# Kernel tuning notes

Measured on AMD Instinct MI355X. Metric: run time of the kernel, lower is better.

## Reference

```python
import jax, jax.numpy as jnp
import numpy as np

B, S, D, E, K = 4, 4096, 2048, 64, 2


def setup_inputs() -> dict:
    key = jax.random.key(0)
    k1, k2 = jax.random.split(key)
    hidden_states = jax.random.normal(k1, (B, S, D), dtype=jnp.float32)
    gate_weight = jax.random.normal(k2, (E, D), dtype=jnp.float32) * 0.02
    return {"hidden_states": hidden_states, "gate_weight": gate_weight}


def reference(hidden_states, gate_weight):
    b, s, d = hidden_states.shape
    e = gate_weight.shape[0]
    n = b * s
    x = hidden_states.reshape(n, d)
    logits = x @ gate_weight.T                                  # [N, E]
    # Original reassigns gate_logits = softmax(gate_logits) in fp32.
    probs = jax.nn.softmax(logits.astype(jnp.float32), axis=-1)  # [N, E]

    top_v, top_i = jax.lax.top_k(probs, K)                       # [N, K]
    top_k_gates = top_v  # normalize_gate_prob_before_dropping=False

    oh = jax.nn.one_hot(top_i, e, dtype=probs.dtype)             # [N, K, E]
    gates = jnp.einsum('nke,nk->ne', oh, top_k_gates)            # scatter of top-k gates

    # Auxiliary losses (training path, use_aux_loss=True)
    gates_mean = gates.mean(axis=0)                              # [E]
    selection_mean = oh.sum(axis=(0, 1)) / n                     # [E]
    load_balancing_loss = (gates_mean * selection_mean).sum() * e
    # NOTE: original computes z-loss on the softmaxed probs (gate_logits was overwritten)
    router_z_loss = (jax.nn.logsumexp(probs, axis=-1) ** 2).mean()

    # torch scatter_ with index [B,S,1,1] only ever writes slot k=0.
    dispatch0 = oh.sum(axis=1).reshape(b, s, e)                  # 1.0 at top-k experts
    combine0 = gates.reshape(b, s, e)
    pad = ((0, 0), (0, 0), (0, 0), (0, K - 1))
    dispatch_tensor = jnp.pad(dispatch0[..., None], pad)         # [B,S,E,K]
    combine_tensor = jnp.pad(combine0[..., None], pad)           # [B,S,E,K]

    return dispatch_tensor, combine_tensor, load_balancing_loss, router_z_loss
```

## Files before the change

### kernel.cpp

```cpp
#include <hip/hip_runtime.h>
#include <hip/hip_bf16.h>
#include <cstddef>

namespace {
constexpr int kD = 2048;
constexpr int kE = 64;
constexpr int kN = 16384;
constexpr size_t kDispatchFloats = (size_t)kN * kE * 2;
constexpr size_t kWsplitOff = 1024;
}

typedef short short8_t __attribute__((ext_vector_type(8)));
typedef float f32x4 __attribute__((ext_vector_type(4)));

__global__ void zero_ws_kernel(float* __restrict__ ws) {
  ws[threadIdx.x] = 0.0f;
}

__device__ __forceinline__ void split3(float f, unsigned short& s1,
                                       unsigned short& s2, unsigned short& s3) {
  __hip_bfloat16 h1 = __float2bfloat16(f);
  float r1 = (f - __bfloat162float(h1)) * 256.0f;
  __hip_bfloat16 h2 = __float2bfloat16(r1);
  float r2 = (r1 - __bfloat162float(h2)) * 256.0f;
  __hip_bfloat16 h3 = __float2bfloat16(r2);
  s1 = __builtin_bit_cast(unsigned short, h1);
  s2 = __builtin_bit_cast(unsigned short, h2);
  s3 = __builtin_bit_cast(unsigned short, h3);
}

__global__ __launch_bounds__(256)
void split_w_kernel(const float* __restrict__ W, unsigned short* __restrict__ img) {
  const int t   = blockIdx.x * 256 + threadIdx.x;
  const int dq  = t >> 12;
  const int c   = (t >> 9) & 7;
  const int row = (t >> 3) & 63;
  const int cs8 = t & 7;
  const int co  = cs8 ^ (row & 7);
  const float* src = W + (size_t)row * kD + dq * 512 + c * 64 + co * 8;
  const float4 v0 = *reinterpret_cast<const float4*>(src);
  const float4 v1 = *reinterpret_cast<const float4*>(src + 4);
  short8_t o1, o2, o3;
  unsigned short s1, s2, s3;
  split3(v0.x, s1, s2, s3); o1[0]=(short)s1; o2[0]=(short)s2; o3[0]=(short)s3;
  split3(v0.y, s1, s2, s3); o1[1]=(short)s1; o2[1]=(short)s2; o3[1]=(short)s3;
  split3(v0.z, s1, s2, s3); o1[2]=(short)s1; o2[2]=(short)s2; o3[2]=(short)s3;
  split3(v0.w, s1, s2, s3); o1[3]=(short)s1; o2[3]=(short)s2; o3[3]=(short)s3;
  split3(v1.x, s1, s2, s3); o1[4]=(short)s1; o2[4]=(short)s2; o3[4]=(short)s3;
  split3(v1.y, s1, s2, s3); o1[5]=(short)s1; o2[5]=(short)s2; o3[5]=(short)s3;
  split3(v1.z, s1, s2, s3); o1[6]=(short)s1; o2[6]=(short)s2; o3[6]=(short)s3;
  split3(v1.w, s1, s2, s3); o1[7]=(short)s1; o2[7]=(short)s2; o3[7]=(short)s3;
  unsigned short* dst = img + (size_t)(dq * 8 + c) * 12288 + row * 64 + cs8 * 8;
  *reinterpret_cast<short8_t*>(dst + 0 * 4096) = o1;
  *reinterpret_cast<short8_t*>(dst + 1 * 4096) = o2;
  *reinterpret_cast<short8_t*>(dst + 2 * 4096) = o3;
}

__device__ __forceinline__ void conv_store8(float4 a, float4 b,
                                            unsigned short (*dst)[64][64],
                                            int row, int seg) {
  short8_t o1, o2, o3;
  unsigned short s1, s2, s3;
  split3(a.x, s1, s2, s3); o1[0]=(short)s1; o2[0]=(short)s2; o3[0]=(short)s3;
  split3(a.y, s1, s2, s3); o1[1]=(short)s1; o2[1]=(short)s2; o3[1]=(short)s3;
  split3(a.z, s1, s2, s3); o1[2]=(short)s1; o2[2]=(short)s2; o3[2]=(short)s3;
  split3(a.w, s1, s2, s3); o1[3]=(short)s1; o2[3]=(short)s2; o3[3]=(short)s3;
  split3(b.x, s1, s2, s3); o1[4]=(short)s1; o2[4]=(short)s2; o3[4]=(short)s3;
  split3(b.y, s1, s2, s3); o1[5]=(short)s1; o2[5]=(short)s2; o3[5]=(short)s3;
  split3(b.z, s1, s2, s3); o1[6]=(short)s1; o2[6]=(short)s2; o3[6]=(short)s3;
  split3(b.w, s1, s2, s3); o1[7]=(short)s1; o2[7]=(short)s2; o3[7]=(short)s3;
  const int col = seg ^ (row & 7);
  *reinterpret_cast<short8_t*>(&dst[0][row][col * 8]) = o1;
  *reinterpret_cast<short8_t*>(&dst[1][row][col * 8]) = o2;
  *reinterpret_cast<short8_t*>(&dst[2][row][col * 8]) = o3;
}

__global__ __launch_bounds__(512)
void logits_kernel(const float* __restrict__ x,
                   const unsigned short* __restrict__ wimg,
                   float* __restrict__ out) {
  __shared__ unsigned short xs[3][64][64];
  __shared__ unsigned short wt[3][64][64];

  const int tid  = threadIdx.x;
  const int lane = tid & 63;
  const int wv   = __builtin_amdgcn_readfirstlane(tid >> 6);
  const int wr   = wv >> 2;
  const int wc   = (wv >> 1) & 1;
  const int kh   = wv & 1;
  const int tile = blockIdx.x & 255;
  const int dq   = blockIdx.x >> 8;
  const int lrow = lane & 15;
  const int lk   = lane >> 4;

  const int row = tid >> 3, seg = tid & 7;
  const float4* __restrict__ bx = reinterpret_cast<const float4*>(x) +
      ((size_t)tile * 64 + row) * 512 + dq * 128 + seg * 2;
  const unsigned short* __restrict__ wbase =
      wimg + (size_t)dq * 8 * 12288 + tid * 8;
  unsigned short* wtf = &wt[0][0][0];

  f32x4 acc0[2][2], acc1[2][2], acc2[2][2];
  const f32x4 z4 = {0.0f, 0.0f, 0.0f, 0.0f};
#pragma unroll
  for (int a = 0; a < 2; ++a)
#pragma unroll
    for (int b = 0; b < 2; ++b) { acc0[a][b] = z4; acc1[a][b] = z4; acc2[a][b] = z4; }

  float4 vx0 = bx[0], vx1 = bx[1];

  for (int c = 0; c < 8; ++c) {
    const unsigned short* wsrc = wbase + (size_t)c * 12288;
#pragma unroll
    for (int i = 0; i < 3; ++i)
      __builtin_amdgcn_global_load_lds(
          (const __attribute__((address_space(1))) void*)(wsrc + i * 4096),
          (__attribute__((address_space(3))) void*)(wtf + i * 4096 + wv * 512),
          16, 0, 0);
    __builtin_amdgcn_sched_barrier(0);
    const float4 xa = vx0, xb = vx1;
    const int cn = (c + 1) & 7;
    vx0 = bx[cn * 16 + 0];
    vx1 = bx[cn * 16 + 1];
    conv_store8(xa, xb, xs, row, seg);
    asm volatile("s_waitcnt vmcnt(2) lgkmcnt(0)" ::: "memory");
    __builtin_amdgcn_sched_barrier(0);
    __builtin_amdgcn_s_barrier();
    __builtin_amdgcn_sched_barrier(0);
    {
      const int kc = kh * 4 + lk;
      short8_t a1[2], a2[2], a3[2], b1[2], b2[2], b3[2];
#pragma unroll
      for (int nt = 0; nt < 2; ++nt) {
        const int e = wc * 32 + nt * 16 + lrow;
        const int cw = (kc ^ (e & 7)) * 8;
        b1[nt] = *reinterpret_cast<const short8_t*>(&wt[0][e][cw]);
        b2[nt] = *reinterpret_cast<const short8_t*>(&wt[1][e][cw]);
        b3[nt] = *reinterpret_cast<const short8_t*>(&wt[2][e][cw]);
      }
#pragma unroll
      for (int mt = 0; mt < 2; ++mt) {
        const int r = wr * 32 + mt * 16 + lrow;
        const int cw = (kc ^ (r & 7)) * 8;
        a1[mt] = *reinterpret_cast<const short8_t*>(&xs[0][r][cw]);
        a2[mt] = *reinterpret_cast<const short8_t*>(&xs[1][r][cw]);
        a3[mt] = *reinterpret_cast<const short8_t*>(&xs[2][r][cw]);
      }
#pragma unroll
      for (int mt = 0; mt < 2; ++mt)
#pragma unroll
        for (int nt = 0; nt < 2; ++nt) {
          acc0[mt][nt] = __builtin_amdgcn_mfma_f32_16x16x32_bf16(a1[mt], b1[nt], acc0[mt][nt], 0, 0, 0);
          acc1[mt][nt] = __builtin_amdgcn_mfma_f32_16x16x32_bf16(a1[mt], b2[nt], acc1[mt][nt], 0, 0, 0);
          acc1[mt][nt] = __builtin_amdgcn_mfma_f32_16x16x32_bf16(a2[mt], b1[nt], acc1[mt][nt], 0, 0, 0);
          acc2[mt][nt] = __builtin_amdgcn_mfma_f32_16x16x32_bf16(a1[mt], b3[nt], acc2[mt][nt], 0, 0, 0);
          acc2[mt][nt] = __builtin_amdgcn_mfma_f32_16x16x32_bf16(a3[mt], b1[nt], acc2[mt][nt], 0, 0, 0);
          acc2[mt][nt] = __builtin_amdgcn_mfma_f32_16x16x32_bf16(a2[mt], b2[nt], acc2[mt][nt], 0, 0, 0);
        }
    }
    __builtin_amdgcn_sched_barrier(0);
    __builtin_amdgcn_s_barrier();
  }

  const float k8 = 1.0f / 256.0f, k16 = 1.0f / 65536.0f;
  float* __restrict__ mbuf = reinterpret_cast<float*>(&xs[0][0][0]);
  if (kh == 1) {
#pragma unroll
    for (int mt = 0; mt < 2; ++mt)
#pragma unroll
      for (int nt = 0; nt < 2; ++nt)
#pragma unroll
        for (int r = 0; r < 4; ++r) {
          const int trow = wr * 32 + mt * 16 + lk * 4 + r;
          const int col  = wc * 32 + nt * 16 + lrow;
          mbuf[trow * 65 + col] =
              acc0[mt][nt][r] + acc1[mt][nt][r] * k8 + acc2[mt][nt][r] * k16;
        }
  }
  __syncthreads();
  if (kh == 0) {
    float* __restrict__ base = out + ((dq < 2) ? (size_t)0 : kDispatchFloats);
#pragma unroll
    for (int mt = 0; mt < 2; ++mt)
#pragma unroll
      for (int r = 0; r < 4; ++r) {
        const int trow = wr * 32 + mt * 16 + lk * 4 + r;
        const size_t n = (size_t)tile * 64 + trow;
        float* __restrict__ dst =
            base + n * 128 + (dq & 1) * 64 + wc * 32 + lrow;
#pragma unroll
        for (int nt = 0; nt < 2; ++nt) {
          const int col = wc * 32 + nt * 16 + lrow;
          dst[nt * 16] = acc0[mt][nt][r] + acc1[mt][nt][r] * k8 +
                         acc2[mt][nt][r] * k16 + mbuf[trow * 65 + col];
        }
      }
  }
}

__global__ __launch_bounds__(256)
void gate_kernel(float* __restrict__ out, float* __restrict__ ws) {
  __shared__ float lg[64][65];
  __shared__ int ti0[64], ti1[64];
  __shared__ float tv0[64], tv1[64], tz2[64];
  const int tid  = threadIdx.x;
  const int tile = blockIdx.x;

  float* __restrict__ outd = out + (size_t)tile * 8192;
  float* __restrict__ outc = out + kDispatchFloats + (size_t)tile * 8192;
  const float4* __restrict__ d4 = reinterpret_cast<const float4*>(outd);
  const float4* __restrict__ c4 = reinterpret_cast<const float4*>(outc);

  const int tq = tid >> 4, q = tid & 15;
#pragma unroll
  for (int k = 0; k < 4; ++k) {
    const int t = k * 16 + tq;
    const float4 a = d4[t * 32 + q];
    const float4 b = d4[t * 32 + 16 + q];
    const float4 c = c4[t * 32 + q];
    const float4 d = c4[t * 32 + 16 + q];
    lg[t][q * 4 + 0] = a.x + b.x + c.x + d.x;
    lg[t][q * 4 + 1] = a.y + b.y + c.y + d.y;
    lg[t][q * 4 + 2] = a.z + b.z + c.z + d.z;
    lg[t][q * 4 + 3] = a.w + b.w + c.w + d.w;
  }
  __syncthreads();

  if (tid < 64) {
    float v0 = -INFINITY, v1 = -INFINITY;
    int i0 = 0, i1 = 0;
    for (int e = 0; e < kE; ++e) {
      const float l = lg[tid][e];
      if (l > v0) { v1 = v0; i1 = i0; v0 = l; i0 = e; }
      else if (l > v1) { v1 = l; i1 = e; }
    }
    const float m = v0;
    float s = 0.0f;
    for (int e = 0; e < kE; ++e) s += __expf(lg[tid][e] - m);
    const float rs = 1.0f / s;
    float zexp = 0.0f;
    for (int e = 0; e < kE; ++e) zexp += __expf(__expf(lg[tid][e] - m) * rs);
    const float z = logf(zexp);
    ti0[tid] = i0; ti1[tid] = i1;
    tv0[tid] = rs;
    tv1[tid] = __expf(v1 - m) * rs;
    tz2[tid] = z * z;
  }
  __syncthreads();

  if (tid < kE) {
    float g = 0.0f, cnt = 0.0f;
    for (int t = 0; t < 64; ++t) {
      if (ti0[t] == tid) { g += tv0[t]; cnt += 1.0f; }
      if (ti1[t] == tid) { g += tv1[t]; cnt += 1.0f; }
    }
    atomicAdd(&ws[tid], g);
    atomicAdd(&ws[kE + tid], cnt);
    float z2 = tz2[tid];
    for (int off = 32; off; off >>= 1) z2 += __shfl_down(z2, off);
    if (tid == 0) atomicAdd(&ws[2 * kE], z2);
  }

  {
    const int t = tid >> 2, sub = tid & 3;
    const int i0 = ti0[t], i1 = ti1[t];
    const float v0 = tv0[t], v1 = tv1[t];
    float4* __restrict__ dp = reinterpret_cast<float4*>(outd) + t * 32;
    float4* __restrict__ cp = reinterpret_cast<float4*>(outc) + t * 32;
#pragma unroll
    for (int j = 0; j < 8; ++j) {
      const int qq = sub * 8 + j;
      const int e0 = qq * 2, e1 = qq * 2 + 1;
      const float d0v = (e0 == i0 || e0 == i1) ? 1.0f : 0.0f;
      const float d1v = (e1 == i0 || e1 == i1) ? 1.0f : 0.0f;
      const float c0 = (e0 == i0) ? v0 : ((e0 == i1) ? v1 : 0.0f);
      const float c1 = (e1 == i0) ? v0 : ((e1 == i1) ? v1 : 0.0f);
      dp[qq] = make_float4(d0v, 0.0f, d1v, 0.0f);
      cp[qq] = make_float4(c0, 0.0f, c1, 0.0f);
    }
  }
}

__global__ void finalize_kernel(const float* __restrict__ ws,
                                float* __restrict__ out) {
  const int e = threadIdx.x;
  float prod = ws[e] * ws[kE + e];
  for (int off = 32; off; off >>= 1) prod += __shfl_down(prod, off);
  if (e == 0) {
    const size_t base = kDispatchFloats * 2;
    const float invN = 1.0f / (float)kN;
    out[base]     = prod * ((float)kE * invN * invN);
    out[base + 1] = ws[2 * kE] * invN;
  }
}

extern "C" void kernel_launch(void* const* d_in, const int* in_sizes, int n_in,
                              void* d_out, int out_size, void* d_ws,
                              size_t ws_size, hipStream_t stream) {
  const float* x = (const float*)d_in[0];
  const float* W = (const float*)d_in[1];
  float* out = (float*)d_out;
  float* ws = (float*)d_ws;
  unsigned short* wimg = (unsigned short*)(ws + kWsplitOff);

  zero_ws_kernel<<<1, 256, 0, stream>>>(ws);
  split_w_kernel<<<64, 256, 0, stream>>>(W, wimg);
  logits_kernel<<<1024, 512, 0, stream>>>(x, wimg, out);
  gate_kernel<<<256, 256, 0, stream>>>(out, ws);
  finalize_kernel<<<1, kE, 0, stream>>>(ws, out);
}
```

Before: 73.29 us.

## Stage fp32 x in LDS, split per wave, single accumulator, fuse zero-init

```diff
diff --git a/kernel.cpp b/kernel.cpp
--- a/kernel.cpp
+++ b/kernel.cpp
@@ -13,25 +13,33 @@
 typedef short short8_t __attribute__((ext_vector_type(8)));
 typedef float f32x4 __attribute__((ext_vector_type(4)));
 
-__global__ void zero_ws_kernel(float* __restrict__ ws) {
-  ws[threadIdx.x] = 0.0f;
-}
-
 __device__ __forceinline__ void split3(float f, unsigned short& s1,
                                        unsigned short& s2, unsigned short& s3) {
   __hip_bfloat16 h1 = __float2bfloat16(f);
-  float r1 = (f - __bfloat162float(h1)) * 256.0f;
+  float r1 = f - __bfloat162float(h1);
   __hip_bfloat16 h2 = __float2bfloat16(r1);
-  float r2 = (r1 - __bfloat162float(h2)) * 256.0f;
+  float r2 = r1 - __bfloat162float(h2);
   __hip_bfloat16 h3 = __float2bfloat16(r2);
   s1 = __builtin_bit_cast(unsigned short, h1);
   s2 = __builtin_bit_cast(unsigned short, h2);
   s3 = __builtin_bit_cast(unsigned short, h3);
 }
 
+__device__ __forceinline__ void split8(f32x4 a, f32x4 b, short8_t& o1,
+                                       short8_t& o2, short8_t& o3) {
+  unsigned short s1, s2, s3;
+#define SP(v, i, j) \
+  split3((v)[i], s1, s2, s3); o1[j]=(short)s1; o2[j]=(short)s2; o3[j]=(short)s3;
+  SP(a, 0, 0) SP(a, 1, 1) SP(a, 2, 2) SP(a, 3, 3)
+  SP(b, 0, 4) SP(b, 1, 5) SP(b, 2, 6) SP(b, 3, 7)
+#undef SP
+}
+
 __global__ __launch_bounds__(256)
-void split_w_kernel(const float* __restrict__ W, unsigned short* __restrict__ img) {
-  const int t   = blockIdx.x * 256 + threadIdx.x;
+void prep_kernel(const float* __restrict__ W, unsigned short* __restrict__ img,
+                 float* __restrict__ ws) {
+  const int t = blockIdx.x * 256 + threadIdx.x;
+  if (t < 512) ws[t] = 0.0f;
   const int dq  = t >> 12;
   const int c   = (t >> 9) & 7;
   const int row = (t >> 3) & 63;
@@ -56,31 +64,14 @@
   *reinterpret_cast<short8_t*>(dst + 2 * 4096) = o3;
 }
 
-__device__ __forceinline__ void conv_store8(float4 a, float4 b,
-                                            unsigned short (*dst)[64][64],
-                                            int row, int seg) {
-  short8_t o1, o2, o3;
-  unsigned short s1, s2, s3;
-  split3(a.x, s1, s2, s3); o1[0]=(short)s1; o2[0]=(short)s2; o3[0]=(short)s3;
-  split3(a.y, s1, s2, s3); o1[1]=(short)s1; o2[1]=(short)s2; o3[1]=(short)s3;
-  split3(a.z, s1, s2, s3); o1[2]=(short)s1; o2[2]=(short)s2; o3[2]=(short)s3;
-  split3(a.w, s1, s2, s3); o1[3]=(short)s1; o2[3]=(short)s2; o3[3]=(short)s3;
-  split3(b.x, s1, s2, s3); o1[4]=(short)s1; o2[4]=(short)s2; o3[4]=(short)s3;
-  split3(b.y, s1, s2, s3); o1[5]=(short)s1; o2[5]=(short)s2; o3[5]=(short)s3;
-  split3(b.z, s1, s2, s3); o1[6]=(short)s1; o2[6]=(short)s2; o3[6]=(short)s3;
-  split3(b.w, s1, s2, s3); o1[7]=(short)s1; o2[7]=(short)s2; o3[7]=(short)s3;
-  const int col = seg ^ (row & 7);
-  *reinterpret_cast<short8_t*>(&dst[0][row][col * 8]) = o1;
-  *reinterpret_cast<short8_t*>(&dst[1][row][col * 8]) = o2;
-  *reinterpret_cast<short8_t*>(&dst[2][row][col * 8]) = o3;
-}
-
-__global__ __launch_bounds__(512)
+__global__ __launch_bounds__(512, 4)
 void logits_kernel(const float* __restrict__ x,
                    const unsigned short* __restrict__ wimg,
                    float* __restrict__ out) {
-  __shared__ unsigned short xs[3][64][64];
-  __shared__ unsigned short wt[3][64][64];
+  __shared__ __attribute__((aligned(16))) unsigned char smem[40960];
+  float* xsf = reinterpret_cast<float*>(smem);
+  unsigned short (*wt)[64][64] =
+      reinterpret_cast<unsigned short (*)[64][64]>(smem + 16384);
 
   const int tid  = threadIdx.x;
   const int lane = tid & 63;
@@ -99,13 +90,12 @@
   const unsigned short* __restrict__ wbase =
       wimg + (size_t)dq * 8 * 12288 + tid * 8;
   unsigned short* wtf = &wt[0][0][0];
-
-  f32x4 acc0[2][2], acc1[2][2], acc2[2][2];
+  const int sc0 = ((2 * seg) ^ (row & 15)) * 4;
+  const int sc1 = ((2 * seg + 1) ^ (row & 15)) * 4;
+
+  f32x4 acc[2][2];
   const f32x4 z4 = {0.0f, 0.0f, 0.0f, 0.0f};
-#pragma unroll
-  for (int a = 0; a < 2; ++a)
-#pragma unroll
-    for (int b = 0; b < 2; ++b) { acc0[a][b] = z4; acc1[a][b] = z4; acc2[a][b] = z4; }
+  acc[0][0] = z4; acc[0][1] = z4; acc[1][0] = z4; acc[1][1] = z4;
 
   float4 vx0 = bx[0], vx1 = bx[1];
 
@@ -122,14 +112,15 @@
     const int cn = (c + 1) & 7;
     vx0 = bx[cn * 16 + 0];
     vx1 = bx[cn * 16 + 1];
-    conv_store8(xa, xb, xs, row, seg);
+    *reinterpret_cast<float4*>(xsf + row * 64 + sc0) = xa;
+    *reinterpret_cast<float4*>(xsf + row * 64 + sc1) = xb;
     asm volatile("s_waitcnt vmcnt(2) lgkmcnt(0)" ::: "memory");
     __builtin_amdgcn_sched_barrier(0);
     __builtin_amdgcn_s_barrier();
     __builtin_amdgcn_sched_barrier(0);
     {
       const int kc = kh * 4 + lk;
-      short8_t a1[2], a2[2], a3[2], b1[2], b2[2], b3[2];
+      short8_t b1[2], b2[2], b3[2];
 #pragma unroll
       for (int nt = 0; nt < 2; ++nt) {
         const int e = wc * 32 + nt * 16 + lrow;
@@ -140,30 +131,29 @@
       }
 #pragma unroll
       for (int mt = 0; mt < 2; ++mt) {
-        const int r = wr * 32 + mt * 16 + lrow;
-        const int cw = (kc ^ (r & 7)) * 8;
-        a1[mt] = *reinterpret_cast<const short8_t*>(&xs[0][r][cw]);
-        a2[mt] = *reinterpret_cast<const short8_t*>(&xs[1][r][cw]);
-        a3[mt] = *reinterpret_cast<const short8_t*>(&xs[2][r][cw]);
+        const int ra = wr * 32 + mt * 16 + lrow;
+        const int ca0 = ((2 * kc) ^ (ra & 15)) * 4;
+        const int ca1 = ((2 * kc + 1) ^ (ra & 15)) * 4;
+        const f32x4 va = *reinterpret_cast<const f32x4*>(xsf + ra * 64 + ca0);
+        const f32x4 vb = *reinterpret_cast<const f32x4*>(xsf + ra * 64 + ca1);
+        short8_t a1, a2, a3;
+        split8(va, vb, a1, a2, a3);
+#pragma unroll
+        for (int nt = 0; nt < 2; ++nt) {
+          acc[mt][nt] = __builtin_amdgcn_mfma_f32_16x16x32_bf16(a1, b1[nt], acc[mt][nt], 0, 0, 0);
+          acc[mt][nt] = __builtin_amdgcn_mfma_f32_16x16x32_bf16(a1, b2[nt], acc[mt][nt], 0, 0, 0);
+          acc[mt][nt] = __builtin_amdgcn_mfma_f32_16x16x32_bf16(a2, b1[nt], acc[mt][nt], 0, 0, 0);
+          acc[mt][nt] = __builtin_amdgcn_mfma_f32_16x16x32_bf16(a1, b3[nt], acc[mt][nt], 0, 0, 0);
+          acc[mt][nt] = __builtin_amdgcn_mfma_f32_16x16x32_bf16(a3, b1[nt], acc[mt][nt], 0, 0, 0);
+          acc[mt][nt] = __builtin_amdgcn_mfma_f32_16x16x32_bf16(a2, b2[nt], acc[mt][nt], 0, 0, 0);
+        }
       }
-#pragma unroll
-      for (int mt = 0; mt < 2; ++mt)
-#pragma unroll
-        for (int nt = 0; nt < 2; ++nt) {
-          acc0[mt][nt] = __builtin_amdgcn_mfma_f32_16x16x32_bf16(a1[mt], b1[nt], acc0[mt][nt], 0, 0, 0);
-          acc1[mt][nt] = __builtin_amdgcn_mfma_f32_16x16x32_bf16(a1[mt], b2[nt], acc1[mt][nt], 0, 0, 0);
-          acc1[mt][nt] = __builtin_amdgcn_mfma_f32_16x16x32_bf16(a2[mt], b1[nt], acc1[mt][nt], 0, 0, 0);
-          acc2[mt][nt] = __builtin_amdgcn_mfma_f32_16x16x32_bf16(a1[mt], b3[nt], acc2[mt][nt], 0, 0, 0);
-          acc2[mt][nt] = __builtin_amdgcn_mfma_f32_16x16x32_bf16(a3[mt], b1[nt], acc2[mt][nt], 0, 0, 0);
-          acc2[mt][nt] = __builtin_amdgcn_mfma_f32_16x16x32_bf16(a2[mt], b2[nt], acc2[mt][nt], 0, 0, 0);
-        }
     }
     __builtin_amdgcn_sched_barrier(0);
     __builtin_amdgcn_s_barrier();
   }
 
-  const float k8 = 1.0f / 256.0f, k16 = 1.0f / 65536.0f;
-  float* __restrict__ mbuf = reinterpret_cast<float*>(&xs[0][0][0]);
+  float* __restrict__ mbuf = reinterpret_cast<float*>(smem + 16384);
   if (kh == 1) {
 #pragma unroll
     for (int mt = 0; mt < 2; ++mt)
@@ -173,8 +163,7 @@
         for (int r = 0; r < 4; ++r) {
           const int trow = wr * 32 + mt * 16 + lk * 4 + r;
           const int col  = wc * 32 + nt * 16 + lrow;
-          mbuf[trow * 65 + col] =
-              acc0[mt][nt][r] + acc1[mt][nt][r] * k8 + acc2[mt][nt][r] * k16;
+          mbuf[trow * 65 + col] = acc[mt][nt][r];
         }
   }
   __syncthreads();
@@ -191,8 +180,7 @@
 #pragma unroll
         for (int nt = 0; nt < 2; ++nt) {
           const int col = wc * 32 + nt * 16 + lrow;
-          dst[nt * 16] = acc0[mt][nt][r] + acc1[mt][nt][r] * k8 +
-                         acc2[mt][nt][r] * k16 + mbuf[trow * 65 + col];
+          dst[nt * 16] = acc[mt][nt][r] + mbuf[trow * 65 + col];
         }
       }
   }
@@ -303,8 +291,7 @@
   float* ws = (float*)d_ws;
   unsigned short* wimg = (unsigned short*)(ws + kWsplitOff);
 
-  zero_ws_kernel<<<1, 256, 0, stream>>>(ws);
-  split_w_kernel<<<64, 256, 0, stream>>>(W, wimg);
+  prep_kernel<<<64, 256, 0, stream>>>(W, wimg, ws);
   logits_kernel<<<1024, 512, 0, stream>>>(x, wimg, out);
   gate_kernel<<<256, 256, 0, stream>>>(out, ws);
   finalize_kernel<<<1, kE, 0, stream>>>(ws, out);
```

Result: no change. 73.54 us (+0.3%).
